# Kernel tuning notes

Measured on AMD Instinct MI355X. Metric: run time of the kernel, lower is better.

The kernel has to match this reference:

```python
import jax, jax.numpy as jnp
import numpy as np

EPS = 1e-5
SHARE = 8  # share_planes

def batchnorm(x, gamma, beta):
    # BatchNorm1d over the point (batch) dimension, training-mode stats
    mu = jnp.mean(x, axis=0, keepdims=True)
    var = jnp.var(x, axis=0, keepdims=True)
    return gamma * (x - mu) * jax.lax.rsqrt(var + EPS) + beta

def setup_inputs() -> dict:
    key = jax.random.key(0)
    ks = jax.random.split(key, 12)
    N, K, C = 100000, 16, 64
    s = 0.05
    return {
        "p": jax.random.normal(ks[0], (N, 3), jnp.float32),
        "x": jax.random.normal(ks[1], (N, C), jnp.float32),
        "knn_idx": jax.random.randint(ks[2], (N, K), 0, N, jnp.int32),
        "W1": jax.random.normal(ks[3], (C, C), jnp.float32) * s,
        "Wv": jax.random.normal(ks[4], (C, C), jnp.float32) * s,
        "Wp1": jax.random.normal(ks[5], (3, C), jnp.float32) * s,
        "Wp2": jax.random.normal(ks[6], (C, C), jnp.float32) * s,
        "Ww": jax.random.normal(ks[7], (C, C // SHARE), jnp.float32) * s,
        "W3": jax.random.normal(ks[8], (C, C), jnp.float32) * s,
        "g1": jnp.ones((C,), jnp.float32), "b1": jnp.zeros((C,), jnp.float32),
        "g2": jnp.ones((C,), jnp.float32), "b2": jnp.zeros((C,), jnp.float32),
        "g3": jnp.ones((C,), jnp.float32), "b3": jnp.zeros((C,), jnp.float32),
    }

def reference(p, x, knn_idx, W1, Wv, Wp1, Wp2, Ww, W3, g1, b1, g2, b2, g3, b3):
    # PointMixerBlock: linear1/bn1 -> intra-set mixing/bn2 -> linear3/bn3 + residual
    identity = x
    h = jax.nn.relu(batchnorm(x @ W1, g1, b1))              # [N, C]
    # --- PointMixer intra-set layer (gather-compute-aggregate) ---
    v = h @ Wv                                               # values [N, C]
    pj = p[knn_idx]                                          # [N, K, 3] neighbor coords
    delta = pj - p[:, None, :]                               # relative positions
    e = jax.nn.relu(delta @ Wp1) @ Wp2                       # pos encoding [N, K, C]
    hj = h[knn_idx]                                          # neighbor feats [N, K, C]
    energy = (hj + e) @ Ww                                   # [N, K, C//SHARE]
    w = jax.nn.softmax(energy, axis=1)                       # mix over K neighbors
    w = jnp.repeat(w, SHARE, axis=2)                         # share weights across channel groups
    mixed = jnp.sum(w * (v[knn_idx] + e), axis=1)            # [N, C]
    # -------------------------------------------------------------
    h = jax.nn.relu(batchnorm(mixed, g2, b2))
    h = batchnorm(h @ W3, g3, b3)
    return jax.nn.relu(h + identity)
```

## Files before the change

kernel.cpp:

```cpp
#include <hip/hip_runtime.h>
#include <hip/hip_fp16.h>

#define EPSV 1e-5f
#define PST 2048
#define GRID_GEMM 1563
#define GRID_MIX  2048
#define GRID_ELT  2048

typedef _Float16 h2_t  __attribute__((ext_vector_type(2)));
typedef __fp16   fp16x2 __attribute__((ext_vector_type(2)));
typedef _Float16 f16x4 __attribute__((ext_vector_type(4)));
typedef _Float16 f16x8 __attribute__((ext_vector_type(8)));
typedef float    f32x4 __attribute__((ext_vector_type(4)));
typedef unsigned short u16;

__device__ __forceinline__ float frelu(float x) { return fmaxf(x, 0.f); }

__device__ __forceinline__ unsigned int pkrtz(float lo, float hi) {
  fp16x2 h = __builtin_amdgcn_cvt_pkrtz(lo, hi);
  return __builtin_bit_cast(unsigned int, h);
}
__device__ __forceinline__ u16 f16b(float x) {
  return (u16)(pkrtz(x, 0.f) & 0xffffu);
}
__device__ __forceinline__ float f16tof(u16 u) {
  return (float)(*reinterpret_cast<const _Float16*>(&u));
}
__device__ __forceinline__ f16x8 mk8(unsigned a, unsigned b, unsigned c, unsigned d) {
  uint4 u; u.x = a; u.y = b; u.z = c; u.w = d;
  return __builtin_bit_cast(f16x8, u);
}
__device__ __forceinline__ f16x4 mk4(unsigned a, unsigned b) {
  uint2 u; u.x = a; u.y = b;
  return __builtin_bit_cast(f16x4, u);
}
__device__ __forceinline__ f32x4 mfma16(f16x8 a, f16x8 b, f32x4 c) {
  return __builtin_amdgcn_mfma_f32_16x16x32_f16(a, b, c, 0, 0, 0);
}
__device__ __forceinline__ f32x4 mfma16k16(f16x4 a, f16x4 b, f32x4 c) {
  return __builtin_amdgcn_mfma_f32_16x16x16f16(a, b, c, 0, 0, 0);
}
__device__ __forceinline__ unsigned relu2(unsigned u) {
  const unsigned m = ((u & 0x80008000u) >> 15) * 0xFFFFu;
  return u & ~m;
}

template<int MODE, bool INF16>
__global__ __launch_bounds__(256, 4) void gemm_mfma_k(
    const void* __restrict__ in, const float* __restrict__ W,
    const float* __restrict__ Ww, const float* __restrict__ ss,
    u16* __restrict__ out16, u16* __restrict__ outw16,
    float* __restrict__ partials, int N,
    const float* __restrict__ Wp2, const float* __restrict__ Wp1,
    uint4* __restrict__ wwf, uint4* __restrict__ wp2f, uint4* __restrict__ w1f)
{
  __shared__ float red[512];
  __shared__ u16 xh[4][16*72];
  const int t = threadIdx.x, lane = t & 63, w = t >> 6;
  const int r16 = lane & 15, q = lane >> 4;

  if (MODE == 0 && blockIdx.x == GRID_GEMM) {
    float* wwl = (float*)&xh[0][0];
    {
      const int a = t >> 2, qq = t & 3;
      float acc[8] = {0,0,0,0,0,0,0,0};
#pragma unroll
      for (int cc = 0; cc < 16; ++cc) {
        const int c = qq*16 + cc;
        const float wv = Wp2[a*64 + c];
#pragma unroll
        for (int g = 0; g < 8; ++g) acc[g] = fmaf(wv, Ww[c*8 + g], acc[g]);
      }
#pragma unroll
      for (int g = 0; g < 8; ++g) {
        acc[g] += __shfl_xor(acc[g], 1);
        acc[g] += __shfl_xor(acc[g], 2);
      }
      if (qq == 0) {
#pragma unroll
        for (int g = 0; g < 8; ++g) wwl[a*8 + g] = acc[g];
      }
    }
    __syncthreads();
    if (t < 128) {
      const int h = t >> 6, l = t & 63, rr = l & 15, qq = l >> 4;
      uint4 u = {0,0,0,0};
      if (rr < 8) {
        u.x = pkrtz(wwl[(32*h+8*qq+0)*8 + rr], wwl[(32*h+8*qq+1)*8 + rr]);
        u.y = pkrtz(wwl[(32*h+8*qq+2)*8 + rr], wwl[(32*h+8*qq+3)*8 + rr]);
        u.z = pkrtz(wwl[(32*h+8*qq+4)*8 + rr], wwl[(32*h+8*qq+5)*8 + rr]);
        u.w = pkrtz(wwl[(32*h+8*qq+6)*8 + rr], wwl[(32*h+8*qq+7)*8 + rr]);
      }
      wwf[t] = u;
    }
    for (int e = t; e < 512; e += 256) {
      const int tt = e >> 7, h = (e >> 6) & 1, l = e & 63;
      const int c = 16*tt + (l & 15), qq = l >> 4;
      const int d0 = 32*h + 8*qq;
      uint4 u;
      u.x = pkrtz(Wp2[(d0+0)*64 + c], Wp2[(d0+1)*64 + c]);
      u.y = pkrtz(Wp2[(d0+2)*64 + c], Wp2[(d0+3)*64 + c]);
      u.z = pkrtz(Wp2[(d0+4)*64 + c], Wp2[(d0+5)*64 + c]);
      u.w = pkrtz(Wp2[(d0+6)*64 + c], Wp2[(d0+7)*64 + c]);
      wp2f[e] = u;
    }
    for (int e = t; e < 384; e += 256) {
      const int r = e >> 7, h = (e >> 6) & 1, l = e & 63, qq = l >> 4;
      const int d0 = 32*h + 8*qq;
      uint4 u;
      u.x = pkrtz(Wp1[r*64 + d0+0], Wp1[r*64 + d0+1]);
      u.y = pkrtz(Wp1[r*64 + d0+2], Wp1[r*64 + d0+3]);
      u.z = pkrtz(Wp1[r*64 + d0+4], Wp1[r*64 + d0+5]);
      u.w = pkrtz(Wp1[r*64 + d0+6], Wp1[r*64 + d0+7]);
      w1f[e] = u;
    }
    return;
  }

  u16* const xw = &xh[w][0];
  f16x8 bw[2][4];
#pragma unroll
  for (int kb = 0; kb < 2; ++kb) {
#pragma unroll
    for (int tt = 0; tt < 4; ++tt) {
      const int kbase = 32*kb + 8*q;
      const int cc = 16*tt + r16;
      unsigned u0 = pkrtz(W[(kbase+0)*64 + cc], W[(kbase+1)*64 + cc]);
      unsigned u1 = pkrtz(W[(kbase+2)*64 + cc], W[(kbase+3)*64 + cc]);
      unsigned u2 = pkrtz(W[(kbase+4)*64 + cc], W[(kbase+5)*64 + cc]);
      unsigned u3 = pkrtz(W[(kbase+6)*64 + cc], W[(kbase+7)*64 + cc]);
      bw[kb][tt] = mk8(u0, u1, u2, u3);
    }
  }
  f16x8 bg[2];
  if (MODE == 1) {
#pragma unroll
    for (int kb = 0; kb < 2; ++kb) {
      const int kbase = 32*kb + 8*q;
      unsigned u[4];
#pragma unroll
      for (int mm = 0; mm < 4; ++mm) {
        float g0 = (r16 < 8) ? Ww[(kbase + 2*mm    )*8 + r16] : 0.f;
        float g1 = (r16 < 8) ? Ww[(kbase + 2*mm + 1)*8 + r16] : 0.f;
        u[mm] = pkrtz(g0, g1);
      }
      bg[kb] = mk8(u[0], u[1], u[2], u[3]);
    }
  }
  float sc4[4], sh4[4];
  if (MODE != 0) {
#pragma unroll
    for (int j = 0; j < 4; ++j) {
      sc4[j] = ss[4*r16 + j];
      sh4[j] = ss[64 + 4*r16 + j];
    }
  }

  float S4[4] = {0,0,0,0}, Q4[4] = {0,0,0,0};
  const int ntiles = (N + 15) >> 4;
  for (int tile = blockIdx.x*4 + w; tile < ntiles; tile += GRID_GEMM*4) {
    const int r0 = tile << 4;
    const bool full = (r0 + 16 <= N);
#pragma unroll
    for (int i = 0; i < 4; ++i) {
      const int row = q + 4*i;
      float4 xv = {0.f, 0.f, 0.f, 0.f};
      const bool rok = full || (r0 + row < N);
      if (rok) {
        if constexpr (INF16) {
          const uint2 u = *(const uint2*)((const u16*)in + (size_t)(r0 + row)*64 + 4*r16);
          const h2_t lo = __builtin_bit_cast(h2_t, u.x);
          const h2_t hi = __builtin_bit_cast(h2_t, u.y);
          xv.x = (float)lo[0]; xv.y = (float)lo[1];
          xv.z = (float)hi[0]; xv.w = (float)hi[1];
        } else {
          xv = *(const float4*)((const float*)in + (size_t)(r0 + row)*64 + 4*r16);
        }
      }
      if (MODE != 0) {
        xv.x = frelu(fmaf(xv.x, sc4[0], sh4[0]));
        xv.y = frelu(fmaf(xv.y, sc4[1], sh4[1]));
        xv.z = frelu(fmaf(xv.z, sc4[2], sh4[2]));
        xv.w = frelu(fmaf(xv.w, sc4[3], sh4[3]));
        if (!rok) { xv.x = 0.f; xv.y = 0.f; xv.z = 0.f; xv.w = 0.f; }
      }
      uint2 u2v; u2v.x = pkrtz(xv.x, xv.y); u2v.y = pkrtz(xv.z, xv.w);
      *(uint2*)(xw + row*72 + 4*r16) = u2v;
    }
    const f16x8 a0 = __builtin_bit_cast(f16x8, *(const uint4*)(xw + r16*72 + 8*q));
    const f16x8 a1 = __builtin_bit_cast(f16x8, *(const uint4*)(xw + r16*72 + 8*q + 32));
    f32x4 acc[4];
#pragma unroll
    for (int tt = 0; tt < 4; ++tt) {
      f32x4 z = {0.f, 0.f, 0.f, 0.f};
      z = mfma16(a0, bw[0][tt], z);
      acc[tt] = mfma16(a1, bw[1][tt], z);
    }
#pragma unroll
    for (int tt = 0; tt < 4; ++tt) {
#pragma unroll
      for (int j = 0; j < 4; ++j) {
        if (full || (r0 + 4*q + j < N))
          out16[(size_t)(r0 + 4*q + j)*64 + 16*tt + r16] = f16b(acc[tt][j]);
      }
      if (MODE != 1) {
        S4[tt] += acc[tt][0] + acc[tt][1] + acc[tt][2] + acc[tt][3];
        Q4[tt] = fmaf(acc[tt][0], acc[tt][0], Q4[tt]);
        Q4[tt] = fmaf(acc[tt][1], acc[tt][1], Q4[tt]);
        Q4[tt] = fmaf(acc[tt][2], acc[tt][2], Q4[tt]);
        Q4[tt] = fmaf(acc[tt][3], acc[tt][3], Q4[tt]);
      }
    }
    if (MODE == 1) {
      f32x4 accw = {0.f, 0.f, 0.f, 0.f};
      accw = mfma16(a0, bg[0], accw);
      accw = mfma16(a1, bg[1], accw);
      if (r16 < 8) {
#pragma unroll
        for (int j = 0; j < 4; ++j) {
          if (full || (r0 + 4*q + j < N))
            outw16[(size_t)(r0 + 4*q + j)*8 + r16] = f16b(accw[j]);
        }
      }
    }
  }
  if (MODE != 1) {
#pragma unroll
    for (int tt = 0; tt < 4; ++tt) {
      S4[tt] += __shfl_xor(S4[tt], 16); S4[tt] += __shfl_xor(S4[tt], 32);
      Q4[tt] += __shfl_xor(Q4[tt], 16); Q4[tt] += __shfl_xor(Q4[tt], 32);
    }
    if (lane < 16) {
#pragma unroll
      for (int tt = 0; tt < 4; ++tt) {
        red[w*128 + tt*16 + lane]      = S4[tt];
        red[w*128 + 64 + tt*16 + lane] = Q4[tt];
      }
    }
    __syncthreads();
    if (t < 64) {
      const float s = red[t] + red[128+t] + red[256+t] + red[384+t];
      const float qq = red[64+t] + red[192+t] + red[320+t] + red[448+t];
      partials[(size_t)t*PST + blockIdx.x]      = s;
      partials[(size_t)(64+t)*PST + blockIdx.x] = qq;
    }
  }
}

__global__ __launch_bounds__(256) void fin_k(const float* __restrict__ partials,
    int nblk, const float* __restrict__ gamma, const float* __restrict__ beta,
    float* __restrict__ ss, float invN)
{
  __shared__ float red[8];
  const int c = blockIdx.x;
  float s = 0.f, q = 0.f;
  for (int i = threadIdx.x; i < nblk; i += 256) {
    s += partials[(size_t)c*PST + i];
    q += partials[(size_t)(64+c)*PST + i];
  }
#pragma unroll
  for (int mk = 1; mk < 64; mk <<= 1) {
    s += __shfl_xor(s, mk);
    q += __shfl_xor(q, mk);
  }
  const int w = threadIdx.x >> 6;
  if ((threadIdx.x & 63) == 0) { red[w*2] = s; red[w*2+1] = q; }
  __syncthreads();
  if (threadIdx.x == 0) {
    const float S = red[0]+red[2]+red[4]+red[6];
    const float Q = red[1]+red[3]+red[5]+red[7];
    const float mean = S*invN;
    const float var  = Q*invN - mean*mean;
    const float scale = gamma[c] * rsqrtf(var + EPSV);
    ss[c] = scale; ss[64+c] = beta[c] - mean*scale;
  }
}

__global__ __launch_bounds__(256, 4) void mixer_k(
    const float* __restrict__ p, const int* __restrict__ knn,
    const u16* __restrict__ v16, const u16* __restrict__ hw16,
    const uint4* __restrict__ wwf, const uint4* __restrict__ wp2f,
    const uint4* __restrict__ w1f,
    u16* __restrict__ mx16, float* __restrict__ partials, int N)
{
  __shared__ float red[512];
  const int t = threadIdx.x, lane = t & 63, w = t >> 6;
  const int r16 = lane & 15, q = lane >> 4, b = r16 >> 3;

  f16x8 wwB[2];
  wwB[0] = __builtin_bit_cast(f16x8, wwf[lane]);
  wwB[1] = __builtin_bit_cast(f16x8, wwf[64 + lane]);
  f16x8 wp2B[8];
#pragma unroll
  for (int e = 0; e < 8; ++e)
    wp2B[e] = __builtin_bit_cast(f16x8, wp2f[e*64 + lane]);
  unsigned w1a[6][4];
#pragma unroll
  for (int e = 0; e < 6; ++e) {
    const uint4 u = w1f[e*64 + lane];
    w1a[e][0] = u.x; w1a[e][1] = u.y; w1a[e][2] = u.z; w1a[e][3] = u.w;
  }

  float ssum = 0.f, sq = 0.f;
  const int nwaves = gridDim.x * 4;

  for (int i = blockIdx.x*4 + w; i < N; i += nwaves) {
    const int4 kn4 = *(const int4*)(knn + (size_t)i*16 + 4*q);
    const int kn[4] = {kn4.x, kn4.y, kn4.z, kn4.w};
    const int jj = knn[(size_t)i*16 + r16];
    u16 vt[4][4];
#pragma unroll
    for (int j = 0; j < 4; ++j) {
      const u16* vp = v16 + (size_t)kn[j]*64 + r16;
#pragma unroll
      for (int tt = 0; tt < 4; ++tt) vt[tt][j] = vp[16*tt];
    }
    u16 hvu[4];
#pragma unroll
    for (int j = 0; j < 4; ++j) hvu[j] = hw16[(size_t)kn[j]*8 + r16];
    const float pix = p[(size_t)i*3], piy = p[(size_t)i*3+1], piz = p[(size_t)i*3+2];
    const float dx = p[(size_t)jj*3]   - pix;
    const float dy = p[(size_t)jj*3+1] - piy;
    const float dz = p[(size_t)jj*3+2] - piz;

    const h2_t dx2 = __builtin_bit_cast(h2_t, pkrtz(dx, dx));
    const h2_t dy2 = __builtin_bit_cast(h2_t, pkrtz(dy, dy));
    const h2_t dz2 = __builtin_bit_cast(h2_t, pkrtz(dz, dz));
    f16x8 eA[2];
#pragma unroll
    for (int h = 0; h < 2; ++h) {
      unsigned eu[4];
#pragma unroll
      for (int mm = 0; mm < 4; ++mm) {
        h2_t acc = dz2 * __builtin_bit_cast(h2_t, w1a[4+h][mm]);
        acc = dy2 * __builtin_bit_cast(h2_t, w1a[2+h][mm]) + acc;
        acc = dx2 * __builtin_bit_cast(h2_t, w1a[0+h][mm]) + acc;
        eu[mm] = relu2(__builtin_bit_cast(unsigned, acc));
      }
      eA[h] = mk8(eu[0], eu[1], eu[2], eu[3]);
    }

    f32x4 en = {0.f, 0.f, 0.f, 0.f};
    en = mfma16(eA[0], wwB[0], en);
    en = mfma16(eA[1], wwB[1], en);
#pragma unroll
    for (int j = 0; j < 4; ++j)
      en[j] += (r16 < 8) ? f16tof(hvu[j]) : 0.f;

    float m = fmaxf(fmaxf(en[0], en[1]), fmaxf(en[2], en[3]));
    m = fmaxf(m, __shfl_xor(m, 16));
    m = fmaxf(m, __shfl_xor(m, 32));
    const float e0 = __expf(en[0]-m), e1 = __expf(en[1]-m);
    const float e2 = __expf(en[2]-m), e3 = __expf(en[3]-m);
    float s = e0 + e1 + e2 + e3;
    s += __shfl_xor(s, 16);
    s += __shfl_xor(s, 32);
    const float rs = 1.f / s;
    const f16x4 aw = mk4(pkrtz(e0*rs, e1*rs), pkrtz(e2*rs, e3*rs));

    float outv = 0.f;
#pragma unroll
    for (int tt = 0; tt < 4; ++tt) {
      f32x4 E = {0.f, 0.f, 0.f, 0.f};
      E = mfma16(eA[0], wp2B[tt*2], E);
      E = mfma16(eA[1], wp2B[tt*2+1], E);
#pragma unroll
      for (int j = 0; j < 4; ++j) E[j] += f16tof(vt[tt][j]);
      const f16x4 bE = mk4(pkrtz(E[0], E[1]), pkrtz(E[2], E[3]));
      f32x4 G = {0.f, 0.f, 0.f, 0.f};
      G = mfma16k16(aw, bE, G);
      const float sel = b ? G[(2*tt+1) & 3] : G[(2*tt) & 3];
      const float val = __shfl(sel, ((tt >= 2) ? 16 : 0) + r16);
      if (q == tt) outv = val;
    }
    mx16[(size_t)i*64 + lane] = f16b(outv);
    ssum += outv; sq = fmaf(outv, outv, sq);
  }
  __syncthreads();
  red[w*128 + lane] = ssum; red[w*128 + 64 + lane] = sq;
  __syncthreads();
  if (t < 64) {
    const float s = red[t] + red[128+t] + red[256+t] + red[384+t];
    const float qv = red[64+t] + red[192+t] + red[320+t] + red[448+t];
    partials[(size_t)t*PST + blockIdx.x]      = s;
    partials[(size_t)(64+t)*PST + blockIdx.x] = qv;
  }
}

__global__ __launch_bounds__(256) void final_k(const u16* __restrict__ y16,
    const float* __restrict__ x, const float* __restrict__ ss,
    float* __restrict__ out, int n4)
{
  __shared__ float sl[128];
  if (threadIdx.x < 128) sl[threadIdx.x] = ss[threadIdx.x];
  __syncthreads();
  for (int idx = blockIdx.x*256 + threadIdx.x; idx < n4; idx += gridDim.x*256) {
    const int cb = (idx & 15) << 2;
    const uint2 yu = *(const uint2*)(y16 + (size_t)idx*4);
    const h2_t ylo = __builtin_bit_cast(h2_t, yu.x);
    const h2_t yhi = __builtin_bit_cast(h2_t, yu.y);
    const float4 xx = ((const float4*)x)[idx];
    float4 o;
    o.x = frelu(fmaf((float)ylo[0], sl[cb],   sl[64+cb])   + xx.x);
    o.y = frelu(fmaf((float)ylo[1], sl[cb+1], sl[64+cb+1]) + xx.y);
    o.z = frelu(fmaf((float)yhi[0], sl[cb+2], sl[64+cb+2]) + xx.z);
    o.w = frelu(fmaf((float)yhi[1], sl[cb+3], sl[64+cb+3]) + xx.w);
    ((float4*)out)[idx] = o;
  }
}

extern "C" void kernel_launch(void* const* d_in, const int* in_sizes, int n_in,
                              void* d_out, int out_size, void* d_ws, size_t ws_size,
                              hipStream_t stream)
{
  (void)n_in; (void)out_size; (void)ws_size;
  const float* p   = (const float*)d_in[0];
  const float* x   = (const float*)d_in[1];
  const int*   knn = (const int*)  d_in[2];
  const float* W1  = (const float*)d_in[3];
  const float* Wv  = (const float*)d_in[4];
  const float* Wp1 = (const float*)d_in[5];
  const float* Wp2 = (const float*)d_in[6];
  const float* Ww  = (const float*)d_in[7];
  const float* W3  = (const float*)d_in[8];
  const float* g1  = (const float*)d_in[9];
  const float* b1  = (const float*)d_in[10];
  const float* g2  = (const float*)d_in[11];
  const float* b2  = (const float*)d_in[12];
  const float* g3  = (const float*)d_in[13];
  const float* b3  = (const float*)d_in[14];
  const int N = in_sizes[0] / 3;
  const float invN = 1.f / (float)N;

  u16* ws16 = (u16*)d_ws;
  u16* y16   = ws16;
  u16* v16   = y16 + (size_t)N*64;
  u16* mx16  = v16 + (size_t)N*64;
  u16* hw16  = mx16 + (size_t)N*64;
  uint4* fr  = (uint4*)(hw16 + (size_t)N*8);
  uint4* wwf  = fr;
  uint4* wp2f = fr + 128;
  uint4* w1f  = fr + 640;
  float* partials = (float*)(fr + 1024);
  float* ss1      = partials + (size_t)128*PST;
  float* ss2      = ss1 + 128;
  float* ss3      = ss2 + 128;

  gemm_mfma_k<0, false><<<GRID_GEMM + 1, 256, 0, stream>>>(
      x, W1, Ww, nullptr, y16, nullptr, partials, N, Wp2, Wp1, wwf, wp2f, w1f);
  fin_k<<<64, 256, 0, stream>>>(partials, GRID_GEMM, g1, b1, ss1, invN);
  gemm_mfma_k<1, true><<<GRID_GEMM, 256, 0, stream>>>(
      y16, Wv, Ww, ss1, v16, hw16, nullptr, N, nullptr, nullptr, nullptr, nullptr, nullptr);
  mixer_k<<<GRID_MIX, 256, 0, stream>>>(p, knn, v16, hw16, wwf, wp2f, w1f, mx16, partials, N);
  fin_k<<<64, 256, 0, stream>>>(partials, GRID_MIX, g2, b2, ss2, invN);
  gemm_mfma_k<2, true><<<GRID_GEMM, 256, 0, stream>>>(
      mx16, W3, nullptr, ss2, y16, nullptr, partials, N, nullptr, nullptr, nullptr, nullptr, nullptr);
  fin_k<<<64, 256, 0, stream>>>(partials, GRID_GEMM, g3, b3, ss3, invN);
  final_k<<<GRID_ELT, 256, 0, stream>>>(y16, x, ss3, (float*)d_out, N*16);
}
```

Measured before the change: 122.2 us.

## Move mixer weight fragments to LDS and raise occupancy target

The mixer kernel no longer keeps the Ww, Wp2 and Wp1 fragments in registers. It stages all 1024 fragment vectors in shared memory once per block and reads them from LDS inside the loop, and the launch bound rises from 4 to 6 blocks per CU to hide gather latency. The value gather now packs pairs of f16 neighbours into 32-bit words and adds v through an extra MFMA instead of per-element float adds. The trade is extra LDS reads and an extra MFMA per channel tile, plus 16KB of LDS per block, which may itself cap occupancy.

```diff
diff --git a/kernel.cpp b/kernel.cpp
--- a/kernel.cpp
+++ b/kernel.cpp
@@ -22,9 +22,6 @@
 }
 __device__ __forceinline__ u16 f16b(float x) {
   return (u16)(pkrtz(x, 0.f) & 0xffffu);
-}
-__device__ __forceinline__ float f16tof(u16 u) {
-  return (float)(*reinterpret_cast<const _Float16*>(&u));
 }
 __device__ __forceinline__ f16x8 mk8(unsigned a, unsigned b, unsigned c, unsigned d) {
   uint4 u; u.x = a; u.y = b; u.z = c; u.w = d;
@@ -276,30 +273,19 @@
   }
 }
 
-__global__ __launch_bounds__(256, 4) void mixer_k(
+__global__ __launch_bounds__(256, 6) void mixer_k(
     const float* __restrict__ p, const int* __restrict__ knn,
     const u16* __restrict__ v16, const u16* __restrict__ hw16,
-    const uint4* __restrict__ wwf, const uint4* __restrict__ wp2f,
-    const uint4* __restrict__ w1f,
+    const uint4* __restrict__ frags,
     u16* __restrict__ mx16, float* __restrict__ partials, int N)
 {
+  __shared__ uint4 cst[1024];
   __shared__ float red[512];
   const int t = threadIdx.x, lane = t & 63, w = t >> 6;
   const int r16 = lane & 15, q = lane >> 4, b = r16 >> 3;
 
-  f16x8 wwB[2];
-  wwB[0] = __builtin_bit_cast(f16x8, wwf[lane]);
-  wwB[1] = __builtin_bit_cast(f16x8, wwf[64 + lane]);
-  f16x8 wp2B[8];
-#pragma unroll
-  for (int e = 0; e < 8; ++e)
-    wp2B[e] = __builtin_bit_cast(f16x8, wp2f[e*64 + lane]);
-  unsigned w1a[6][4];
-#pragma unroll
-  for (int e = 0; e < 6; ++e) {
-    const uint4 u = w1f[e*64 + lane];
-    w1a[e][0] = u.x; w1a[e][1] = u.y; w1a[e][2] = u.z; w1a[e][3] = u.w;
-  }
+  for (int e = t; e < 1024; e += 256) cst[e] = frags[e];
+  __syncthreads();
 
   float ssum = 0.f, sq = 0.f;
   const int nwaves = gridDim.x * 4;
@@ -308,20 +294,24 @@
     const int4 kn4 = *(const int4*)(knn + (size_t)i*16 + 4*q);
     const int kn[4] = {kn4.x, kn4.y, kn4.z, kn4.w};
     const int jj = knn[(size_t)i*16 + r16];
-    u16 vt[4][4];
-#pragma unroll
-    for (int j = 0; j < 4; ++j) {
-      const u16* vp = v16 + (size_t)kn[j]*64 + r16;
-#pragma unroll
-      for (int tt = 0; tt < 4; ++tt) vt[tt][j] = vp[16*tt];
-    }
-    u16 hvu[4];
+    unsigned vtp[4][2];
+#pragma unroll
+    for (int tt = 0; tt < 4; ++tt) {
+      const unsigned v0 = v16[(size_t)kn[0]*64 + 16*tt + r16];
+      const unsigned v1 = v16[(size_t)kn[1]*64 + 16*tt + r16];
+      const unsigned v2 = v16[(size_t)kn[2]*64 + 16*tt + r16];
+      const unsigned v3 = v16[(size_t)kn[3]*64 + 16*tt + r16];
+      vtp[tt][0] = v0 | (v1 << 16);
+      vtp[tt][1] = v2 | (v3 << 16);
+    }
+    unsigned hvu[4];
 #pragma unroll
     for (int j = 0; j < 4; ++j) hvu[j] = hw16[(size_t)kn[j]*8 + r16];
-    const float pix = p[(size_t)i*3], piy = p[(size_t)i*3+1], piz = p[(size_t)i*3+2];
-    const float dx = p[(size_t)jj*3]   - pix;
-    const float dy = p[(size_t)jj*3+1] - piy;
-    const float dz = p[(size_t)jj*3+2] - piz;
+    const float2 pj2 = *(const float2*)(p + (size_t)jj*3);
+    const float pjz  = p[(size_t)jj*3 + 2];
+    const float dx = pj2.x - p[(size_t)i*3];
+    const float dy = pj2.y - p[(size_t)i*3+1];
+    const float dz = pjz   - p[(size_t)i*3+2];
 
     const h2_t dx2 = __builtin_bit_cast(h2_t, pkrtz(dx, dx));
     const h2_t dy2 = __builtin_bit_cast(h2_t, pkrtz(dy, dy));
@@ -329,23 +319,29 @@
     f16x8 eA[2];
 #pragma unroll
     for (int h = 0; h < 2; ++h) {
+      const uint4 wx = cst[640 + h*64 + lane];
+      const uint4 wy = cst[640 + (2+h)*64 + lane];
+      const uint4 wz = cst[640 + (4+h)*64 + lane];
       unsigned eu[4];
+      const unsigned* wxp = &wx.x; const unsigned* wyp = &wy.x; const unsigned* wzp = &wz.x;
 #pragma unroll
       for (int mm = 0; mm < 4; ++mm) {
-        h2_t acc = dz2 * __builtin_bit_cast(h2_t, w1a[4+h][mm]);
-        acc = dy2 * __builtin_bit_cast(h2_t, w1a[2+h][mm]) + acc;
-        acc = dx2 * __builtin_bit_cast(h2_t, w1a[0+h][mm]) + acc;
+        h2_t acc = dz2 * __builtin_bit_cast(h2_t, wzp[mm]);
+        acc = dy2 * __builtin_bit_cast(h2_t, wyp[mm]) + acc;
+        acc = dx2 * __builtin_bit_cast(h2_t, wxp[mm]) + acc;
         eu[mm] = relu2(__builtin_bit_cast(unsigned, acc));
       }
       eA[h] = mk8(eu[0], eu[1], eu[2], eu[3]);
     }
 
     f32x4 en = {0.f, 0.f, 0.f, 0.f};
-    en = mfma16(eA[0], wwB[0], en);
-    en = mfma16(eA[1], wwB[1], en);
-#pragma unroll
-    for (int j = 0; j < 4; ++j)
-      en[j] += (r16 < 8) ? f16tof(hvu[j]) : 0.f;
+    en = mfma16(eA[0], __builtin_bit_cast(f16x8, cst[lane]), en);
+    en = mfma16(eA[1], __builtin_bit_cast(f16x8, cst[64 + lane]), en);
+#pragma unroll
+    for (int j = 0; j < 4; ++j) {
+      const h2_t hv = __builtin_bit_cast(h2_t, hvu[j]);
+      en[j] += (r16 < 8) ? (float)hv[0] : 0.f;
+    }
 
     float m = fmaxf(fmaxf(en[0], en[1]), fmaxf(en[2], en[3]));
     m = fmaxf(m, __shfl_xor(m, 16));
@@ -362,12 +358,12 @@
 #pragma unroll
     for (int tt = 0; tt < 4; ++tt) {
       f32x4 E = {0.f, 0.f, 0.f, 0.f};
-      E = mfma16(eA[0], wp2B[tt*2], E);
-      E = mfma16(eA[1], wp2B[tt*2+1], E);
-#pragma unroll
-      for (int j = 0; j < 4; ++j) E[j] += f16tof(vt[tt][j]);
+      E = mfma16(eA[0], __builtin_bit_cast(f16x8, cst[128 + (tt*2)*64 + lane]), E);
+      E = mfma16(eA[1], __builtin_bit_cast(f16x8, cst[128 + (tt*2+1)*64 + lane]), E);
       const f16x4 bE = mk4(pkrtz(E[0], E[1]), pkrtz(E[2], E[3]));
+      const f16x4 bV = mk4(vtp[tt][0], vtp[tt][1]);
       f32x4 G = {0.f, 0.f, 0.f, 0.f};
+      G = mfma16k16(aw, bV, G);
       G = mfma16k16(aw, bE, G);
       const float sel = b ? G[(2*tt+1) & 3] : G[(2*tt) & 3];
       const float val = __shfl(sel, ((tt >= 2) ? 16 : 0) + r16);
@@ -451,7 +447,7 @@
   fin_k<<<64, 256, 0, stream>>>(partials, GRID_GEMM, g1, b1, ss1, invN);
   gemm_mfma_k<1, true><<<GRID_GEMM, 256, 0, stream>>>(
       y16, Wv, Ww, ss1, v16, hw16, nullptr, N, nullptr, nullptr, nullptr, nullptr, nullptr);
-  mixer_k<<<GRID_MIX, 256, 0, stream>>>(p, knn, v16, hw16, wwf, wp2f, w1f, mx16, partials, N);
+  mixer_k<<<GRID_MIX, 256, 0, stream>>>(p, knn, v16, hw16, fr, mx16, partials, N);
   fin_k<<<64, 256, 0, stream>>>(partials, GRID_MIX, g2, b2, ss2, invN);
   gemm_mfma_k<2, true><<<GRID_GEMM, 256, 0, stream>>>(
       mx16, W3, nullptr, ss2, y16, nullptr, partials, N, nullptr, nullptr, nullptr, nullptr, nullptr);
```

Measured after the change: 282.0 us. +130.8%, slower.

## Store v in interleaved row layout for vectorized neighbor gathers

Applied to the files above, without the earlier changes.

The V-projection GEMM now writes each row's four column groups as one packed 8-byte store, using a permuted layout where lane r16 owns channels r16, r16+16, r16+32, r16+48. The mixer gathers each neighbor's v with a single uint2 load instead of four scalar 16-bit loads, and repacks them with bit operations. The v term is no longer added to E in fp32; it goes through a separate MFMA against the softmax weights. Aiming at fewer gather instructions and wider memory transactions, at the cost of an extra MFMA per tile and v being summed through a separate fp16 operand.

```diff
diff --git a/kernel.cpp b/kernel.cpp
--- a/kernel.cpp
+++ b/kernel.cpp
@@ -196,14 +196,25 @@
       z = mfma16(a0, bw[0][tt], z);
       acc[tt] = mfma16(a1, bw[1][tt], z);
     }
-#pragma unroll
-    for (int tt = 0; tt < 4; ++tt) {
+    if (MODE == 1) {
 #pragma unroll
       for (int j = 0; j < 4; ++j) {
-        if (full || (r0 + 4*q + j < N))
-          out16[(size_t)(r0 + 4*q + j)*64 + 16*tt + r16] = f16b(acc[tt][j]);
-      }
-      if (MODE != 1) {
+        const int row = r0 + 4*q + j;
+        if (full || row < N) {
+          uint2 st;
+          st.x = pkrtz(acc[0][j], acc[1][j]);
+          st.y = pkrtz(acc[2][j], acc[3][j]);
+          *(uint2*)(out16 + (size_t)row*64 + r16*4) = st;
+        }
+      }
+    } else {
+#pragma unroll
+      for (int tt = 0; tt < 4; ++tt) {
+#pragma unroll
+        for (int j = 0; j < 4; ++j) {
+          if (full || (r0 + 4*q + j < N))
+            out16[(size_t)(r0 + 4*q + j)*64 + 16*tt + r16] = f16b(acc[tt][j]);
+        }
         S4[tt] += acc[tt][0] + acc[tt][1] + acc[tt][2] + acc[tt][3];
         Q4[tt] = fmaf(acc[tt][0], acc[tt][0], Q4[tt]);
         Q4[tt] = fmaf(acc[tt][1], acc[tt][1], Q4[tt]);
@@ -279,8 +290,7 @@
 __global__ __launch_bounds__(256, 4) void mixer_k(
     const float* __restrict__ p, const int* __restrict__ knn,
     const u16* __restrict__ v16, const u16* __restrict__ hw16,
-    const uint4* __restrict__ wwf, const uint4* __restrict__ wp2f,
-    const uint4* __restrict__ w1f,
+    const uint4* __restrict__ frags,
     u16* __restrict__ mx16, float* __restrict__ partials, int N)
 {
   __shared__ float red[512];
@@ -288,16 +298,16 @@
   const int r16 = lane & 15, q = lane >> 4, b = r16 >> 3;
 
   f16x8 wwB[2];
-  wwB[0] = __builtin_bit_cast(f16x8, wwf[lane]);
-  wwB[1] = __builtin_bit_cast(f16x8, wwf[64 + lane]);
+  wwB[0] = __builtin_bit_cast(f16x8, frags[lane]);
+  wwB[1] = __builtin_bit_cast(f16x8, frags[64 + lane]);
   f16x8 wp2B[8];
 #pragma unroll
   for (int e = 0; e < 8; ++e)
-    wp2B[e] = __builtin_bit_cast(f16x8, wp2f[e*64 + lane]);
+    wp2B[e] = __builtin_bit_cast(f16x8, frags[128 + e*64 + lane]);
   unsigned w1a[6][4];
 #pragma unroll
   for (int e = 0; e < 6; ++e) {
-    const uint4 u = w1f[e*64 + lane];
+    const uint4 u = frags[640 + e*64 + lane];
     w1a[e][0] = u.x; w1a[e][1] = u.y; w1a[e][2] = u.z; w1a[e][3] = u.w;
   }
 
@@ -308,13 +318,10 @@
     const int4 kn4 = *(const int4*)(knn + (size_t)i*16 + 4*q);
     const int kn[4] = {kn4.x, kn4.y, kn4.z, kn4.w};
     const int jj = knn[(size_t)i*16 + r16];
-    u16 vt[4][4];
-#pragma unroll
-    for (int j = 0; j < 4; ++j) {
-      const u16* vp = v16 + (size_t)kn[j]*64 + r16;
-#pragma unroll
-      for (int tt = 0; tt < 4; ++tt) vt[tt][j] = vp[16*tt];
-    }
+    uint2 vu[4];
+#pragma unroll
+    for (int j = 0; j < 4; ++j)
+      vu[j] = *(const uint2*)(v16 + (size_t)kn[j]*64 + r16*4);
     u16 hvu[4];
 #pragma unroll
     for (int j = 0; j < 4; ++j) hvu[j] = hw16[(size_t)kn[j]*8 + r16];
@@ -322,6 +329,16 @@
     const float dx = p[(size_t)jj*3]   - pix;
     const float dy = p[(size_t)jj*3+1] - piy;
     const float dz = p[(size_t)jj*3+2] - piz;
+
+    unsigned vtp[4][2];
+    vtp[0][0] = (vu[0].x & 0xffffu) | (vu[1].x << 16);
+    vtp[1][0] = (vu[0].x >> 16)     | (vu[1].x & 0xffff0000u);
+    vtp[2][0] = (vu[0].y & 0xffffu) | (vu[1].y << 16);
+    vtp[3][0] = (vu[0].y >> 16)     | (vu[1].y & 0xffff0000u);
+    vtp[0][1] = (vu[2].x & 0xffffu) | (vu[3].x << 16);
+    vtp[1][1] = (vu[2].x >> 16)     | (vu[3].x & 0xffff0000u);
+    vtp[2][1] = (vu[2].y & 0xffffu) | (vu[3].y << 16);
+    vtp[3][1] = (vu[2].y >> 16)     | (vu[3].y & 0xffff0000u);
 
     const h2_t dx2 = __builtin_bit_cast(h2_t, pkrtz(dx, dx));
     const h2_t dy2 = __builtin_bit_cast(h2_t, pkrtz(dy, dy));
@@ -364,10 +381,10 @@
       f32x4 E = {0.f, 0.f, 0.f, 0.f};
       E = mfma16(eA[0], wp2B[tt*2], E);
       E = mfma16(eA[1], wp2B[tt*2+1], E);
-#pragma unroll
-      for (int j = 0; j < 4; ++j) E[j] += f16tof(vt[tt][j]);
       const f16x4 bE = mk4(pkrtz(E[0], E[1]), pkrtz(E[2], E[3]));
+      const f16x4 bV = mk4(vtp[tt][0], vtp[tt][1]);
       f32x4 G = {0.f, 0.f, 0.f, 0.f};
+      G = mfma16k16(aw, bV, G);
       G = mfma16k16(aw, bE, G);
       const float sel = b ? G[(2*tt+1) & 3] : G[(2*tt) & 3];
       const float val = __shfl(sel, ((tt >= 2) ? 16 : 0) + r16);
@@ -451,7 +468,7 @@
   fin_k<<<64, 256, 0, stream>>>(partials, GRID_GEMM, g1, b1, ss1, invN);
   gemm_mfma_k<1, true><<<GRID_GEMM, 256, 0, stream>>>(
       y16, Wv, Ww, ss1, v16, hw16, nullptr, N, nullptr, nullptr, nullptr, nullptr, nullptr);
-  mixer_k<<<GRID_MIX, 256, 0, stream>>>(p, knn, v16, hw16, wwf, wp2f, w1f, mx16, partials, N);
+  mixer_k<<<GRID_MIX, 256, 0, stream>>>(p, knn, v16, hw16, fr, mx16, partials, N);
   fin_k<<<64, 256, 0, stream>>>(partials, GRID_MIX, g2, b2, ss2, invN);
   gemm_mfma_k<2, true><<<GRID_GEMM, 256, 0, stream>>>(
       mx16, W3, nullptr, ss2, y16, nullptr, partials, N, nullptr, nullptr, nullptr, nullptr, nullptr);
```

After: 121.7 us. No clear change (-0.3%).
